# Performance work log

Hardware: AMD Instinct MI355X
Metric: run time of the kernel (lower is better)

Reference implementation:

```python
import jax, jax.numpy as jnp
import numpy as np
from jax import lax

HIDDEN = 256
CONV = 128
DIST = 11
GRID = DIST + 1            # 12
N_STAB = DIST * DIST - 1   # 120
N_LAYERS = 2
DILATIONS = tuple(min(2 ** i, DIST) for i in range(N_LAYERS))  # (1, 2)
EPS = 1e-5

# row-major placement of the first N_STAB grid cells (matches _build_grid_maps)
ROWS = jnp.arange(N_STAB) // GRID
COLS = jnp.arange(N_STAB) % GRID


def setup_inputs() -> dict:
    key = jax.random.key(0)
    ks = jax.random.split(key, 12)
    s_in = 1.0 / np.sqrt(HIDDEN)
    s_cv = 1.0 / np.sqrt(CONV * 9)
    s_out = 1.0 / np.sqrt(CONV)
    return {
        "x": jax.random.normal(ks[0], (4096, N_STAB, HIDDEN), jnp.float32),
        "W_in": jax.random.uniform(ks[1], (HIDDEN, CONV), jnp.float32, -s_in, s_in),
        "b_in": jax.random.uniform(ks[2], (CONV,), jnp.float32, -s_in, s_in),
        "conv_w": jax.random.uniform(ks[3], (N_LAYERS, CONV, CONV, 3, 3), jnp.float32, -s_cv, s_cv),
        "conv_b": jax.random.uniform(ks[4], (N_LAYERS, CONV), jnp.float32, -s_cv, s_cv),
        "bn_g": jnp.ones((N_LAYERS, CONV), jnp.float32),
        "bn_b": jnp.zeros((N_LAYERS, CONV), jnp.float32),
        "W_out": jax.random.uniform(ks[5], (CONV, HIDDEN), jnp.float32, -s_out, s_out),
        "b_out": jax.random.uniform(ks[6], (HIDDEN,), jnp.float32, -s_out, s_out),
        "ln_g": jnp.ones((HIDDEN,), jnp.float32),
        "ln_b": jnp.zeros((HIDDEN,), jnp.float32),
    }


def _dilated_conv(g, w, b, dil):
    # g: [B, C, G, G], w: [O, I, 3, 3]
    y = lax.conv_general_dilated(
        g, w, window_strides=(1, 1),
        padding=((dil, dil), (dil, dil)),
        rhs_dilation=(dil, dil),
        dimension_numbers=("NCHW", "OIHW", "NCHW"))
    return y + b[None, :, None, None]


def _batchnorm_train(y, gamma, beta):
    # training-mode BN: batch stats over (N, H, W), biased variance
    mean = jnp.mean(y, axis=(0, 2, 3), keepdims=True)
    var = jnp.mean(jnp.square(y - mean), axis=(0, 2, 3), keepdims=True)
    yhat = (y - mean) * lax.rsqrt(var + EPS)
    return yhat * gamma[None, :, None, None] + beta[None, :, None, None]


def reference(x, W_in, b_in, conv_w, conv_b, bn_g, bn_b, W_out, b_out, ln_g, ln_b):
    B = x.shape[0]
    # proj_in: [B, S, H] -> [B, S, C]
    h = jnp.einsum("bsh,hc->bsc", x, W_in) + b_in
    # scatter to grid: [B, C, G, G]
    grid = jnp.zeros((B, CONV, GRID, GRID), dtype=h.dtype)
    grid = grid.at[:, :, ROWS, COLS].set(jnp.transpose(h, (0, 2, 1)))
    for i, dil in enumerate(DILATIONS):
        y = _dilated_conv(grid, conv_w[i], conv_b[i], dil)
        grid = grid + jax.nn.relu(_batchnorm_train(y, bn_g[i], bn_b[i]))
    # gather back: [B, S, C]
    h = jnp.transpose(grid[:, :, ROWS, COLS], (0, 2, 1))
    # proj_out + residual + LayerNorm
    h = jnp.einsum("bsc,ch->bsh", h, W_out) + b_out
    z = x + h
    mu = jnp.mean(z, axis=-1, keepdims=True)
    var = jnp.mean(jnp.square(z - mu), axis=-1, keepdims=True)
    return (z - mu) * lax.rsqrt(var + EPS) * ln_g + ln_b
```

## Files before the change

kernel.cpp:

```cpp
#include <hip/hip_runtime.h>

typedef __attribute__((ext_vector_type(8))) unsigned short u16x8;
typedef __attribute__((ext_vector_type(4))) unsigned short u16x4;
typedef __attribute__((ext_vector_type(8))) __bf16 bf16x8;
typedef __attribute__((ext_vector_type(4))) float f32x4;

#define DEVINL __device__ __forceinline__

DEVINL f32x4 MF(u16x8 a, u16x8 b, f32x4 c) {
  return __builtin_amdgcn_mfma_f32_16x16x32_bf16(
      __builtin_bit_cast(bf16x8, a), __builtin_bit_cast(bf16x8, b), c, 0, 0, 0);
}
DEVINL unsigned short f2b(float f) {
  unsigned u = __builtin_bit_cast(unsigned, f);
  u += 0x7FFFu + ((u >> 16) & 1u);
  return (unsigned short)(u >> 16);
}
DEVINL float b2f(unsigned short h) {
  unsigned u = ((unsigned)h) << 16;
  return __builtin_bit_cast(float, u);
}

__global__ void k_prep(const float* __restrict__ W_in, const float* __restrict__ conv_w,
                       const float* __restrict__ W_out, unsigned short* __restrict__ Wt_in,
                       unsigned short* __restrict__ Wc, unsigned short* __restrict__ Wt_out) {
  int t = blockIdx.x * 256 + threadIdx.x;
  if (t < 128 * 256) { int c = t >> 8, h = t & 255; Wt_in[t] = f2b(W_in[h * 128 + c]); }
  if (t < 256 * 128) { int h = t >> 7, c = t & 127; Wt_out[t] = f2b(W_out[c * 256 + h]); }
  for (int i = t; i < 2 * 9 * 128 * 128; i += 65536) {
    int ii = i & 127, o = (i >> 7) & 127, rest = i >> 14;
    int kk = rest % 9, L = rest / 9;
    Wc[i] = f2b(conv_w[(size_t)((L * 128 + o) * 128 + ii) * 9 + kk]);
  }
}

__global__ __launch_bounds__(256) void k_proj_in(
    const float* __restrict__ x, const unsigned short* __restrict__ Wt_in,
    const float* __restrict__ b_in, unsigned short* __restrict__ gridb) {
  __shared__ unsigned short Xb[128 * 256];
  char* XB = (char*)Xb;
  const int b = blockIdx.x;
  const float* xb = x + (size_t)b * 120 * 256;

  for (int idx = threadIdx.x; idx < (120 * 256) / 4; idx += 256) {
    int row = idx >> 6, col = (idx & 63) << 2;
    f32x4 v = *(const f32x4*)(xb + row * 256 + col);
    u16x4 h = { f2b(v[0]), f2b(v[1]), f2b(v[2]), f2b(v[3]) };
    *(u16x4*)(XB + row * 512 + ((col * 2) ^ ((row & 7) << 4))) = h;
  }
  for (int idx = threadIdx.x; idx < (8 * 256) / 4; idx += 256) {
    int row = 120 + (idx >> 6), col = (idx & 63) << 2;
    u16x4 zz = {0, 0, 0, 0};
    *(u16x4*)(XB + row * 512 + ((col * 2) ^ ((row & 7) << 4))) = zz;
  }
  __syncthreads();

  const int l = threadIdx.x & 63, hi = l >> 4, lo = l & 15, w = threadIdx.x >> 6;
  const f32x4 Z = {0.f, 0.f, 0.f, 0.f};
  f32x4 acc[2][8];
#pragma unroll
  for (int a = 0; a < 2; ++a)
#pragma unroll
    for (int n = 0; n < 8; ++n) acc[a][n] = Z;

  const unsigned short* A0 = Wt_in + (w * 32 + lo) * 256;
  const unsigned short* A1 = A0 + 16 * 256;
#pragma unroll
  for (int ks = 0; ks < 8; ++ks) {
    const int kb = ks * 32 + hi * 8;
    u16x8 a0 = *(const u16x8*)(A0 + kb);
    u16x8 a1 = *(const u16x8*)(A1 + kb);
#pragma unroll
    for (int nt = 0; nt < 8; ++nt) {
      int row = nt * 16 + lo;
      u16x8 bf = *(const u16x8*)(XB + row * 512 + ((kb * 2) ^ ((row & 7) << 4)));
      acc[0][nt] = MF(a0, bf, acc[0][nt]);
      acc[1][nt] = MF(a1, bf, acc[1][nt]);
    }
  }

  unsigned short* gb = gridb + (size_t)b * 128 * 144;
#pragma unroll
  for (int am = 0; am < 2; ++am)
#pragma unroll
    for (int r = 0; r < 4; ++r) {
      const int crow = w * 32 + am * 16 + hi * 4 + r;
      const float bias = b_in[crow];
#pragma unroll
      for (int nt = 0; nt < 8; ++nt) {
        int s = nt * 16 + lo;
        if (s < 120) gb[crow * 144 + s] = f2b(acc[am][nt][r] + bias);
      }
    }
  for (int idx = threadIdx.x; idx < 128 * 24; idx += 256) {
    int c = idx / 24, p = idx - c * 24;
    gb[c * 144 + 120 + p] = 0;
  }
}

__global__ __launch_bounds__(256) void k_conv(
    unsigned short* __restrict__ gridb, unsigned short* __restrict__ ybuf,
    const float* __restrict__ statsP, const unsigned short* __restrict__ WcL,
    const float* __restrict__ convbL, float* __restrict__ partials,
    int dil, int writeback) {
  __shared__ unsigned short Gt[145 * 128];
  char* GT = (char*)Gt;
  const int b = blockIdx.x;
  unsigned short* gbp = gridb + (size_t)b * 128 * 144;
  unsigned short* ybp = ybuf + (size_t)b * 128 * 144;

  for (int idx = threadIdx.x; idx < 128 * 18; idx += 256) {
    int c = idx / 18;
    int p0 = (idx - c * 18) * 8;
    u16x8 g = *(const u16x8*)(gbp + c * 144 + p0);
    if (statsP) {
      u16x8 yv = *(const u16x8*)(ybp + c * 144 + p0);
      float a = statsP[c], bb = statsP[128 + c];
#pragma unroll
      for (int j = 0; j < 8; ++j)
        g[j] = f2b(b2f(g[j]) + fmaxf(0.f, b2f(yv[j]) * a + bb));
      if (writeback) *(u16x8*)(gbp + c * 144 + p0) = g;
    }
#pragma unroll
    for (int j = 0; j < 8; ++j) {
      int p = p0 + j;
      *(unsigned short*)(GT + p * 256 + ((c * 2) ^ ((p & 7) << 4))) = g[j];
    }
  }
  if (threadIdx.x < 64) *(unsigned*)(GT + 144 * 256 + threadIdx.x * 4) = 0u;
  __syncthreads();

  const int l = threadIdx.x & 63, hi = l >> 4, lo = l & 15, w = threadIdx.x >> 6;
  const f32x4 Z = {0.f, 0.f, 0.f, 0.f};
  f32x4 acc[2][9];
#pragma unroll
  for (int a = 0; a < 2; ++a)
#pragma unroll
    for (int n = 0; n < 9; ++n) acc[a][n] = Z;

  int pr[9], pc[9];
#pragma unroll
  for (int nt = 0; nt < 9; ++nt) {
    int p = nt * 16 + lo;
    pr[nt] = p / 12;
    pc[nt] = p - pr[nt] * 12;
  }

  for (int off = 0; off < 9; ++off) {
    const int dh = (off / 3 - 1) * dil, dw = (off % 3 - 1) * dil;
    int rb[9], sz[9];
#pragma unroll
    for (int nt = 0; nt < 9; ++nt) {
      int r2 = pr[nt] + dh, c2 = pc[nt] + dw;
      bool ok = ((unsigned)r2 < 12u) && ((unsigned)c2 < 12u);
      int ps = ok ? (r2 * 12 + c2) : 144;
      rb[nt] = ps * 256;
      sz[nt] = (ps & 7) << 4;
    }
    const unsigned short* Ao = WcL + off * (128 * 128);
#pragma unroll
    for (int ks = 0; ks < 4; ++ks) {
      const int kb = ks * 32 + hi * 8;
      u16x8 a0 = *(const u16x8*)(Ao + (w * 32 + lo) * 128 + kb);
      u16x8 a1 = *(const u16x8*)(Ao + (w * 32 + 16 + lo) * 128 + kb);
#pragma unroll
      for (int nt = 0; nt < 9; ++nt) {
        u16x8 bf = *(const u16x8*)(GT + rb[nt] + ((kb * 2) ^ sz[nt]));
        acc[0][nt] = MF(a0, bf, acc[0][nt]);
        acc[1][nt] = MF(a1, bf, acc[1][nt]);
      }
    }
  }

#pragma unroll
  for (int am = 0; am < 2; ++am)
#pragma unroll
    for (int r = 0; r < 4; ++r) {
      const int orow = w * 32 + am * 16 + hi * 4 + r;
      const float bias = convbL[orow];
      float s1 = 0.f, s2 = 0.f;
#pragma unroll
      for (int nt = 0; nt < 9; ++nt) {
        float yv = acc[am][nt][r] + bias;
        s1 += yv; s2 += yv * yv;
        ybp[orow * 144 + nt * 16 + lo] = f2b(yv);
      }
#pragma unroll
      for (int m = 1; m < 16; m <<= 1) { s1 += __shfl_xor(s1, m); s2 += __shfl_xor(s2, m); }
      if (lo == 0) {
        partials[(size_t)orow * 4096 + b] = s1;
        partials[(size_t)(128 + orow) * 4096 + b] = s2;
      }
    }
}

__global__ void k_stats(const float* __restrict__ partials, const float* __restrict__ bn_g,
                        const float* __restrict__ bn_b, float* __restrict__ statsL, float invN) {
  const int c = blockIdx.x, t = threadIdx.x;
  float s1 = 0.f, s2 = 0.f;
  const float* p1 = partials + (size_t)c * 4096;
  const float* p2 = partials + (size_t)(128 + c) * 4096;
  for (int j = t; j < 4096; j += 256) { s1 += p1[j]; s2 += p2[j]; }
#pragma unroll
  for (int m = 1; m < 64; m <<= 1) { s1 += __shfl_xor(s1, m); s2 += __shfl_xor(s2, m); }
  __shared__ float r1[4], r2[4];
  if ((t & 63) == 0) { r1[t >> 6] = s1; r2[t >> 6] = s2; }
  __syncthreads();
  if (t == 0) {
    float S1 = r1[0] + r1[1] + r1[2] + r1[3];
    float S2 = r2[0] + r2[1] + r2[2] + r2[3];
    float mean = S1 * invN;
    float var = fmaxf(S2 * invN - mean * mean, 0.f);
    float a = bn_g[c] * rsqrtf(var + 1e-5f);
    statsL[c] = a;
    statsL[128 + c] = bn_b[c] - mean * a;
  }
}

__global__ __launch_bounds__(256) void k_out(
    const unsigned short* __restrict__ gridb, const unsigned short* __restrict__ ybuf,
    const float* __restrict__ statsP, const unsigned short* __restrict__ Wt_out,
    const float* __restrict__ b_out, const float* __restrict__ x,
    const float* __restrict__ ln_g, const float* __restrict__ ln_b,
    float* __restrict__ out) {
  __shared__ unsigned short Gs[128 * 128];
  char* GT = (char*)Gs;
  const int b = blockIdx.x;
  const unsigned short* gbp = gridb + (size_t)b * 128 * 144;
  const unsigned short* ybp = ybuf + (size_t)b * 128 * 144;

  for (int idx = threadIdx.x; idx < 128 * 15; idx += 256) {
    int c = idx / 15;
    int p0 = (idx - c * 15) * 8;
    u16x8 g = *(const u16x8*)(gbp + c * 144 + p0);
    u16x8 yv = *(const u16x8*)(ybp + c * 144 + p0);
    float a = statsP[c], bb = statsP[128 + c];
#pragma unroll
    for (int j = 0; j < 8; ++j) {
      float v = b2f(g[j]) + fmaxf(0.f, b2f(yv[j]) * a + bb);
      int s = p0 + j;
      *(unsigned short*)(GT + s * 256 + ((c * 2) ^ ((s & 7) << 4))) = f2b(v);
    }
  }
  for (int idx = threadIdx.x; idx < 512; idx += 256)
    *(unsigned*)(GT + 120 * 256 + idx * 4) = 0u;
  __syncthreads();

  const int l = threadIdx.x & 63, hi = l >> 4, lo = l & 15, w = threadIdx.x >> 6;
  const f32x4 Z = {0.f, 0.f, 0.f, 0.f};
  f32x4 acc[2][16];
#pragma unroll
  for (int a = 0; a < 2; ++a)
#pragma unroll
    for (int n = 0; n < 16; ++n) acc[a][n] = Z;

#pragma unroll
  for (int ks = 0; ks < 4; ++ks) {
    const int kb = ks * 32 + hi * 8;
    const int r0 = w * 32 + lo, r1 = r0 + 16;
    u16x8 a0 = *(const u16x8*)(GT + r0 * 256 + ((kb * 2) ^ ((r0 & 7) << 4)));
    u16x8 a1 = *(const u16x8*)(GT + r1 * 256 + ((kb * 2) ^ ((r1 & 7) << 4)));
#pragma unroll
    for (int nt = 0; nt < 16; ++nt) {
      u16x8 bf = *(const u16x8*)(Wt_out + (nt * 16 + lo) * 128 + kb);
      acc[0][nt] = MF(a0, bf, acc[0][nt]);
      acc[1][nt] = MF(a1, bf, acc[1][nt]);
    }
  }

  const float* xb = x + (size_t)b * 120 * 256;
  float* ob = out + (size_t)b * 120 * 256;
#pragma unroll
  for (int am = 0; am < 2; ++am)
#pragma unroll
    for (int r = 0; r < 4; ++r) {
      const int row = w * 32 + am * 16 + hi * 4 + r;
      if (row < 120) {
        float z[16];
        float s1 = 0.f, s2 = 0.f;
#pragma unroll
        for (int nt = 0; nt < 16; ++nt) {
          const int col = nt * 16 + lo;
          float v = acc[am][nt][r] + b_out[col] + xb[row * 256 + col];
          z[nt] = v; s1 += v; s2 += v * v;
        }
#pragma unroll
        for (int m = 1; m < 16; m <<= 1) { s1 += __shfl_xor(s1, m); s2 += __shfl_xor(s2, m); }
        const float mu = s1 * (1.f / 256.f);
        const float var = fmaxf(s2 * (1.f / 256.f) - mu * mu, 0.f);
        const float rs = rsqrtf(var + 1e-5f);
#pragma unroll
        for (int nt = 0; nt < 16; ++nt) {
          const int col = nt * 16 + lo;
          ob[row * 256 + col] = (z[nt] - mu) * rs * ln_g[col] + ln_b[col];
        }
      }
    }
}

extern "C" void kernel_launch(void* const* d_in, const int* in_sizes, int n_in,
                              void* d_out, int out_size, void* d_ws, size_t ws_size,
                              hipStream_t stream) {
  (void)in_sizes; (void)n_in; (void)out_size; (void)ws_size;
  const float* x      = (const float*)d_in[0];
  const float* W_in   = (const float*)d_in[1];
  const float* b_in   = (const float*)d_in[2];
  const float* conv_w = (const float*)d_in[3];
  const float* conv_b = (const float*)d_in[4];
  const float* bn_g   = (const float*)d_in[5];
  const float* bn_b   = (const float*)d_in[6];
  const float* W_out  = (const float*)d_in[7];
  const float* b_out  = (const float*)d_in[8];
  const float* ln_g   = (const float*)d_in[9];
  const float* ln_b   = (const float*)d_in[10];

  char* ws = (char*)d_ws;
  size_t off = 0;
  auto alloc = [&](size_t bytes) { char* p = ws + off; off = (off + bytes + 255) & ~(size_t)255; return p; };
  unsigned short* Wt_in  = (unsigned short*)alloc(128 * 256 * 2);
  unsigned short* Wc     = (unsigned short*)alloc(2 * 9 * 128 * 128 * 2);
  unsigned short* Wt_out = (unsigned short*)alloc(256 * 128 * 2);
  float* stats           = (float*)alloc(2 * 256 * 4);
  float* partials        = (float*)alloc((size_t)256 * 4096 * 4);
  unsigned short* gridb  = (unsigned short*)alloc((size_t)4096 * 128 * 144 * 2);
  unsigned short* ybuf   = (unsigned short*)alloc((size_t)4096 * 128 * 144 * 2);

  const float invN = 1.f / (4096.f * 144.f);

  k_prep<<<256, 256, 0, stream>>>(W_in, conv_w, W_out, Wt_in, Wc, Wt_out);
  k_proj_in<<<4096, 256, 0, stream>>>(x, Wt_in, b_in, gridb);
  k_conv<<<4096, 256, 0, stream>>>(gridb, ybuf, nullptr, Wc, conv_b, partials, 1, 0);
  k_stats<<<128, 256, 0, stream>>>(partials, bn_g, bn_b, stats, invN);
  k_conv<<<4096, 256, 0, stream>>>(gridb, ybuf, stats, Wc + 9 * 128 * 128, conv_b + 128, partials, 2, 1);
  k_stats<<<128, 256, 0, stream>>>(partials, bn_g + 128, bn_b + 128, stats + 256, invN);
  k_out<<<4096, 256, 0, stream>>>(gridb, ybuf, stats + 256, Wt_out, b_out, x, ln_g, ln_b, (float*)d_out);
}
```

Baseline: 1.218 ms.

## Fuse proj_in with first conv and switch grid buffers to position-major layout

Merges the input projection into the first conv kernel so the projected grid stays in shared memory instead of being written out and read back. The grid and conv-output buffers change from channel-major to position-major [144][128], which allows vectorized 16-byte loads and stores in the BN/ReLU prologues. The conv MFMA operands are swapped so that positions form the M dimension, and bf16 conversion now uses the hardware cast. The cost is a more complex fused kernel and possible extra register pressure, and the strided 2-byte y stores remain scattered.

```diff
diff --git a/kernel.cpp b/kernel.cpp
--- a/kernel.cpp
+++ b/kernel.cpp
@@ -1,7 +1,6 @@
 #include <hip/hip_runtime.h>
 
 typedef __attribute__((ext_vector_type(8))) unsigned short u16x8;
-typedef __attribute__((ext_vector_type(4))) unsigned short u16x4;
 typedef __attribute__((ext_vector_type(8))) __bf16 bf16x8;
 typedef __attribute__((ext_vector_type(4))) float f32x4;
 
@@ -12,9 +11,7 @@
       __builtin_bit_cast(bf16x8, a), __builtin_bit_cast(bf16x8, b), c, 0, 0, 0);
 }
 DEVINL unsigned short f2b(float f) {
-  unsigned u = __builtin_bit_cast(unsigned, f);
-  u += 0x7FFFu + ((u >> 16) & 1u);
-  return (unsigned short)(u >> 16);
+  return __builtin_bit_cast(unsigned short, (__bf16)f);
 }
 DEVINL float b2f(unsigned short h) {
   unsigned u = ((unsigned)h) << 16;
@@ -34,164 +31,190 @@
   }
 }
 
-__global__ __launch_bounds__(256) void k_proj_in(
-    const float* __restrict__ x, const unsigned short* __restrict__ Wt_in,
-    const float* __restrict__ b_in, unsigned short* __restrict__ gridb) {
-  __shared__ unsigned short Xb[128 * 256];
-  char* XB = (char*)Xb;
-  const int b = blockIdx.x;
-  const float* xb = x + (size_t)b * 120 * 256;
-
-  for (int idx = threadIdx.x; idx < (120 * 256) / 4; idx += 256) {
-    int row = idx >> 6, col = (idx & 63) << 2;
-    f32x4 v = *(const f32x4*)(xb + row * 256 + col);
-    u16x4 h = { f2b(v[0]), f2b(v[1]), f2b(v[2]), f2b(v[3]) };
-    *(u16x4*)(XB + row * 512 + ((col * 2) ^ ((row & 7) << 4))) = h;
-  }
-  for (int idx = threadIdx.x; idx < (8 * 256) / 4; idx += 256) {
-    int row = 120 + (idx >> 6), col = (idx & 63) << 2;
-    u16x4 zz = {0, 0, 0, 0};
-    *(u16x4*)(XB + row * 512 + ((col * 2) ^ ((row & 7) << 4))) = zz;
-  }
-  __syncthreads();
-
-  const int l = threadIdx.x & 63, hi = l >> 4, lo = l & 15, w = threadIdx.x >> 6;
+DEVINL void conv_body(const char* GT, const unsigned short* __restrict__ WcL,
+                      const float* __restrict__ convbL, int dil,
+                      unsigned short* __restrict__ ybp, float* __restrict__ partials,
+                      int b, int w, int hi, int lo) {
   const f32x4 Z = {0.f, 0.f, 0.f, 0.f};
-  f32x4 acc[2][8];
-#pragma unroll
-  for (int a = 0; a < 2; ++a)
-#pragma unroll
-    for (int n = 0; n < 8; ++n) acc[a][n] = Z;
-
-  const unsigned short* A0 = Wt_in + (w * 32 + lo) * 256;
-  const unsigned short* A1 = A0 + 16 * 256;
-#pragma unroll
-  for (int ks = 0; ks < 8; ++ks) {
-    const int kb = ks * 32 + hi * 8;
-    u16x8 a0 = *(const u16x8*)(A0 + kb);
-    u16x8 a1 = *(const u16x8*)(A1 + kb);
-#pragma unroll
-    for (int nt = 0; nt < 8; ++nt) {
-      int row = nt * 16 + lo;
-      u16x8 bf = *(const u16x8*)(XB + row * 512 + ((kb * 2) ^ ((row & 7) << 4)));
-      acc[0][nt] = MF(a0, bf, acc[0][nt]);
-      acc[1][nt] = MF(a1, bf, acc[1][nt]);
-    }
-  }
-
-  unsigned short* gb = gridb + (size_t)b * 128 * 144;
-#pragma unroll
-  for (int am = 0; am < 2; ++am)
-#pragma unroll
-    for (int r = 0; r < 4; ++r) {
-      const int crow = w * 32 + am * 16 + hi * 4 + r;
-      const float bias = b_in[crow];
-#pragma unroll
-      for (int nt = 0; nt < 8; ++nt) {
-        int s = nt * 16 + lo;
-        if (s < 120) gb[crow * 144 + s] = f2b(acc[am][nt][r] + bias);
-      }
-    }
-  for (int idx = threadIdx.x; idx < 128 * 24; idx += 256) {
-    int c = idx / 24, p = idx - c * 24;
-    gb[c * 144 + 120 + p] = 0;
-  }
-}
-
-__global__ __launch_bounds__(256) void k_conv(
-    unsigned short* __restrict__ gridb, unsigned short* __restrict__ ybuf,
-    const float* __restrict__ statsP, const unsigned short* __restrict__ WcL,
-    const float* __restrict__ convbL, float* __restrict__ partials,
-    int dil, int writeback) {
-  __shared__ unsigned short Gt[145 * 128];
-  char* GT = (char*)Gt;
-  const int b = blockIdx.x;
-  unsigned short* gbp = gridb + (size_t)b * 128 * 144;
-  unsigned short* ybp = ybuf + (size_t)b * 128 * 144;
-
-  for (int idx = threadIdx.x; idx < 128 * 18; idx += 256) {
-    int c = idx / 18;
-    int p0 = (idx - c * 18) * 8;
-    u16x8 g = *(const u16x8*)(gbp + c * 144 + p0);
-    if (statsP) {
-      u16x8 yv = *(const u16x8*)(ybp + c * 144 + p0);
-      float a = statsP[c], bb = statsP[128 + c];
-#pragma unroll
-      for (int j = 0; j < 8; ++j)
-        g[j] = f2b(b2f(g[j]) + fmaxf(0.f, b2f(yv[j]) * a + bb));
-      if (writeback) *(u16x8*)(gbp + c * 144 + p0) = g;
-    }
-#pragma unroll
-    for (int j = 0; j < 8; ++j) {
-      int p = p0 + j;
-      *(unsigned short*)(GT + p * 256 + ((c * 2) ^ ((p & 7) << 4))) = g[j];
-    }
-  }
-  if (threadIdx.x < 64) *(unsigned*)(GT + 144 * 256 + threadIdx.x * 4) = 0u;
-  __syncthreads();
-
-  const int l = threadIdx.x & 63, hi = l >> 4, lo = l & 15, w = threadIdx.x >> 6;
-  const f32x4 Z = {0.f, 0.f, 0.f, 0.f};
-  f32x4 acc[2][9];
-#pragma unroll
-  for (int a = 0; a < 2; ++a)
-#pragma unroll
-    for (int n = 0; n < 9; ++n) acc[a][n] = Z;
+  f32x4 acc[9][2];
+#pragma unroll
+  for (int mt = 0; mt < 9; ++mt) { acc[mt][0] = Z; acc[mt][1] = Z; }
 
   int pr[9], pc[9];
 #pragma unroll
-  for (int nt = 0; nt < 9; ++nt) {
-    int p = nt * 16 + lo;
-    pr[nt] = p / 12;
-    pc[nt] = p - pr[nt] * 12;
+  for (int mt = 0; mt < 9; ++mt) {
+    int p = mt * 16 + lo;
+    pr[mt] = p / 12;
+    pc[mt] = p - pr[mt] * 12;
   }
 
   for (int off = 0; off < 9; ++off) {
     const int dh = (off / 3 - 1) * dil, dw = (off % 3 - 1) * dil;
     int rb[9], sz[9];
 #pragma unroll
-    for (int nt = 0; nt < 9; ++nt) {
-      int r2 = pr[nt] + dh, c2 = pc[nt] + dw;
+    for (int mt = 0; mt < 9; ++mt) {
+      int r2 = pr[mt] + dh, c2 = pc[mt] + dw;
       bool ok = ((unsigned)r2 < 12u) && ((unsigned)c2 < 12u);
       int ps = ok ? (r2 * 12 + c2) : 144;
-      rb[nt] = ps * 256;
-      sz[nt] = (ps & 7) << 4;
+      rb[mt] = ps * 256;
+      sz[mt] = (ps & 7) << 4;
     }
     const unsigned short* Ao = WcL + off * (128 * 128);
 #pragma unroll
     for (int ks = 0; ks < 4; ++ks) {
       const int kb = ks * 32 + hi * 8;
-      u16x8 a0 = *(const u16x8*)(Ao + (w * 32 + lo) * 128 + kb);
-      u16x8 a1 = *(const u16x8*)(Ao + (w * 32 + 16 + lo) * 128 + kb);
-#pragma unroll
-      for (int nt = 0; nt < 9; ++nt) {
-        u16x8 bf = *(const u16x8*)(GT + rb[nt] + ((kb * 2) ^ sz[nt]));
-        acc[0][nt] = MF(a0, bf, acc[0][nt]);
-        acc[1][nt] = MF(a1, bf, acc[1][nt]);
+      u16x8 b0 = *(const u16x8*)(Ao + (w * 32 + lo) * 128 + kb);
+      u16x8 b1 = *(const u16x8*)(Ao + (w * 32 + 16 + lo) * 128 + kb);
+#pragma unroll
+      for (int mt = 0; mt < 9; ++mt) {
+        u16x8 a = *(const u16x8*)(GT + rb[mt] + ((kb * 2) ^ sz[mt]));
+        acc[mt][0] = MF(a, b0, acc[mt][0]);
+        acc[mt][1] = MF(a, b1, acc[mt][1]);
       }
     }
   }
 
-#pragma unroll
-  for (int am = 0; am < 2; ++am)
+  const float bias0 = convbL[w * 32 + lo], bias1 = convbL[w * 32 + 16 + lo];
+  float s1a = 0.f, s2a = 0.f, s1b = 0.f, s2b = 0.f;
+#pragma unroll
+  for (int mt = 0; mt < 9; ++mt)
 #pragma unroll
     for (int r = 0; r < 4; ++r) {
-      const int orow = w * 32 + am * 16 + hi * 4 + r;
-      const float bias = convbL[orow];
-      float s1 = 0.f, s2 = 0.f;
-#pragma unroll
-      for (int nt = 0; nt < 9; ++nt) {
-        float yv = acc[am][nt][r] + bias;
-        s1 += yv; s2 += yv * yv;
-        ybp[orow * 144 + nt * 16 + lo] = f2b(yv);
+      const int p = mt * 16 + hi * 4 + r;
+      float ya = acc[mt][0][r] + bias0;
+      float yb = acc[mt][1][r] + bias1;
+      s1a += ya; s2a += ya * ya; s1b += yb; s2b += yb * yb;
+      ybp[p * 128 + w * 32 + lo]      = f2b(ya);
+      ybp[p * 128 + w * 32 + 16 + lo] = f2b(yb);
+    }
+  s1a += __shfl_xor(s1a, 16); s1a += __shfl_xor(s1a, 32);
+  s2a += __shfl_xor(s2a, 16); s2a += __shfl_xor(s2a, 32);
+  s1b += __shfl_xor(s1b, 16); s1b += __shfl_xor(s1b, 32);
+  s2b += __shfl_xor(s2b, 16); s2b += __shfl_xor(s2b, 32);
+  if (hi == 0) {
+    const int o0 = w * 32 + lo;
+    partials[(size_t)o0 * 4096 + b]              = s1a;
+    partials[(size_t)(128 + o0) * 4096 + b]      = s2a;
+    partials[(size_t)(o0 + 16) * 4096 + b]       = s1b;
+    partials[(size_t)(128 + o0 + 16) * 4096 + b] = s2b;
+  }
+}
+
+__global__ __launch_bounds__(256) void k_in(
+    const float* __restrict__ x, const unsigned short* __restrict__ Wt_in,
+    const float* __restrict__ b_in, const unsigned short* __restrict__ Wc0,
+    const float* __restrict__ convb0, unsigned short* __restrict__ gridb,
+    unsigned short* __restrict__ ybuf, float* __restrict__ partials) {
+  __shared__ unsigned short Gt[145 * 128];
+  char* GT = (char*)Gt;
+  const int b = blockIdx.x, t = threadIdx.x;
+  const int l = t & 63, hi = l >> 4, lo = l & 15, w = t >> 6;
+  const float* xb = x + (size_t)b * 120 * 256;
+
+  const f32x4 Z = {0.f, 0.f, 0.f, 0.f};
+  f32x4 acc[2][8];
+#pragma unroll
+  for (int mi = 0; mi < 2; ++mi)
+#pragma unroll
+    for (int cn = 0; cn < 8; ++cn) acc[mi][cn] = Z;
+
+#pragma unroll
+  for (int ks = 0; ks < 8; ++ks) {
+    const int kb = ks * 32 + hi * 8;
+    u16x8 af[2];
+#pragma unroll
+    for (int mi = 0; mi < 2; ++mi) {
+      int s = w * 32 + mi * 16 + lo;
+      s = s < 120 ? s : 119;
+      const float* px = xb + s * 256 + kb;
+      f32x4 v0 = *(const f32x4*)px;
+      f32x4 v1 = *(const f32x4*)(px + 4);
+      u16x8 a;
+#pragma unroll
+      for (int j = 0; j < 4; ++j) { a[j] = f2b(v0[j]); a[4 + j] = f2b(v1[j]); }
+      af[mi] = a;
+    }
+#pragma unroll
+    for (int cn = 0; cn < 8; ++cn) {
+      u16x8 bf = *(const u16x8*)(Wt_in + (cn * 16 + lo) * 256 + kb);
+      acc[0][cn] = MF(af[0], bf, acc[0][cn]);
+      acc[1][cn] = MF(af[1], bf, acc[1][cn]);
+    }
+  }
+
+  float binr[8];
+#pragma unroll
+  for (int cn = 0; cn < 8; ++cn) binr[cn] = b_in[cn * 16 + lo];
+
+#pragma unroll
+  for (int mi = 0; mi < 2; ++mi)
+#pragma unroll
+    for (int r = 0; r < 4; ++r) {
+      const int s = w * 32 + mi * 16 + hi * 4 + r;
+      if (s < 120) {
+        const int sw = (s & 7) << 4;
+#pragma unroll
+        for (int cn = 0; cn < 8; ++cn) {
+          const int cb = (cn * 16 + lo) * 2;
+          *(unsigned short*)(GT + s * 256 + (cb ^ sw)) = f2b(acc[mi][cn][r] + binr[cn]);
+        }
       }
-#pragma unroll
-      for (int m = 1; m < 16; m <<= 1) { s1 += __shfl_xor(s1, m); s2 += __shfl_xor(s2, m); }
-      if (lo == 0) {
-        partials[(size_t)orow * 4096 + b] = s1;
-        partials[(size_t)(128 + orow) * 4096 + b] = s2;
-      }
-    }
+    }
+  {
+    u16x8 zz = {0, 0, 0, 0, 0, 0, 0, 0};
+    for (int idx = t; idx < 25 * 16; idx += 256) {
+      int row = 120 + (idx >> 4), ch = (idx & 15) << 4;
+      *(u16x8*)(GT + row * 256 + (ch ^ ((row & 7) << 4))) = zz;
+    }
+  }
+  __syncthreads();
+
+  unsigned short* gbp = gridb + (size_t)b * 144 * 128;
+  for (int idx = t; idx < 144 * 16; idx += 256) {
+    int row = idx >> 4, ch = (idx & 15) << 4;
+    u16x8 v = *(const u16x8*)(GT + row * 256 + (ch ^ ((row & 7) << 4)));
+    *(u16x8*)(gbp + row * 128 + ((idx & 15) << 3)) = v;
+  }
+
+  conv_body(GT, Wc0, convb0, 1, ybuf + (size_t)b * 144 * 128, partials, b, w, hi, lo);
+}
+
+__global__ __launch_bounds__(256) void k_conv2(
+    unsigned short* __restrict__ gridb, unsigned short* __restrict__ ybuf,
+    const float* __restrict__ statsP, const unsigned short* __restrict__ WcL,
+    const float* __restrict__ convbL, float* __restrict__ partials) {
+  __shared__ unsigned short Gt[145 * 128];
+  char* GT = (char*)Gt;
+  const int b = blockIdx.x, t = threadIdx.x;
+  unsigned short* gbp = gridb + (size_t)b * 144 * 128;
+  unsigned short* ybp = ybuf + (size_t)b * 144 * 128;
+  const int c0 = (t & 15) * 8, prow = t >> 4;
+  const f32x4 a0 = *(const f32x4*)(statsP + c0);
+  const f32x4 a1 = *(const f32x4*)(statsP + c0 + 4);
+  const f32x4 g0 = *(const f32x4*)(statsP + 128 + c0);
+  const f32x4 g1 = *(const f32x4*)(statsP + 128 + c0 + 4);
+
+#pragma unroll
+  for (int it = 0; it < 9; ++it) {
+    const int p = prow + 16 * it;
+    u16x8 g = *(const u16x8*)(gbp + p * 128 + c0);
+    u16x8 y = *(const u16x8*)(ybp + p * 128 + c0);
+    u16x8 o;
+#pragma unroll
+    for (int j = 0; j < 4; ++j) {
+      o[j]     = f2b(b2f(g[j])     + fmaxf(0.f, b2f(y[j])     * a0[j] + g0[j]));
+      o[4 + j] = f2b(b2f(g[4 + j]) + fmaxf(0.f, b2f(y[4 + j]) * a1[j] + g1[j]));
+    }
+    *(u16x8*)(gbp + p * 128 + c0) = o;
+    *(u16x8*)(GT + p * 256 + ((c0 * 2) ^ ((p & 7) << 4))) = o;
+  }
+  if (t < 16) {
+    u16x8 zz = {0, 0, 0, 0, 0, 0, 0, 0};
+    *(u16x8*)(GT + 144 * 256 + t * 16) = zz;
+  }
+  __syncthreads();
+
+  conv_body(GT, WcL, convbL, 2, ybp, partials, b, t >> 6, (t & 63) >> 4, t & 15);
 }
 
 __global__ void k_stats(const float* __restrict__ partials, const float* __restrict__ bn_g,
@@ -225,63 +248,68 @@
     float* __restrict__ out) {
   __shared__ unsigned short Gs[128 * 128];
   char* GT = (char*)Gs;
-  const int b = blockIdx.x;
-  const unsigned short* gbp = gridb + (size_t)b * 128 * 144;
-  const unsigned short* ybp = ybuf + (size_t)b * 128 * 144;
-
-  for (int idx = threadIdx.x; idx < 128 * 15; idx += 256) {
-    int c = idx / 15;
-    int p0 = (idx - c * 15) * 8;
-    u16x8 g = *(const u16x8*)(gbp + c * 144 + p0);
-    u16x8 yv = *(const u16x8*)(ybp + c * 144 + p0);
-    float a = statsP[c], bb = statsP[128 + c];
-#pragma unroll
-    for (int j = 0; j < 8; ++j) {
-      float v = b2f(g[j]) + fmaxf(0.f, b2f(yv[j]) * a + bb);
-      int s = p0 + j;
-      *(unsigned short*)(GT + s * 256 + ((c * 2) ^ ((s & 7) << 4))) = f2b(v);
-    }
-  }
-  for (int idx = threadIdx.x; idx < 512; idx += 256)
-    *(unsigned*)(GT + 120 * 256 + idx * 4) = 0u;
+  const int b = blockIdx.x, t = threadIdx.x;
+  const unsigned short* gbp = gridb + (size_t)b * 144 * 128;
+  const unsigned short* ybp = ybuf + (size_t)b * 144 * 128;
+  const int c0 = (t & 15) * 8, prow = t >> 4;
+  const f32x4 a0 = *(const f32x4*)(statsP + c0);
+  const f32x4 a1 = *(const f32x4*)(statsP + c0 + 4);
+  const f32x4 g0 = *(const f32x4*)(statsP + 128 + c0);
+  const f32x4 g1 = *(const f32x4*)(statsP + 128 + c0 + 4);
+
+#pragma unroll
+  for (int it = 0; it < 8; ++it) {
+    const int p = prow + 16 * it;
+    u16x8 o = {0, 0, 0, 0, 0, 0, 0, 0};
+    if (p < 120) {
+      u16x8 g = *(const u16x8*)(gbp + p * 128 + c0);
+      u16x8 y = *(const u16x8*)(ybp + p * 128 + c0);
+#pragma unroll
+      for (int j = 0; j < 4; ++j) {
+        o[j]     = f2b(b2f(g[j])     + fmaxf(0.f, b2f(y[j])     * a0[j] + g0[j]));
+        o[4 + j] = f2b(b2f(g[4 + j]) + fmaxf(0.f, b2f(y[4 + j]) * a1[j] + g1[j]));
+      }
+    }
+    *(u16x8*)(GT + p * 256 + ((c0 * 2) ^ ((p & 7) << 4))) = o;
+  }
   __syncthreads();
 
-  const int l = threadIdx.x & 63, hi = l >> 4, lo = l & 15, w = threadIdx.x >> 6;
+  const int l = t & 63, hi = l >> 4, lo = l & 15, w = t >> 6;
   const f32x4 Z = {0.f, 0.f, 0.f, 0.f};
   f32x4 acc[2][16];
 #pragma unroll
-  for (int a = 0; a < 2; ++a)
-#pragma unroll
-    for (int n = 0; n < 16; ++n) acc[a][n] = Z;
+  for (int mi = 0; mi < 2; ++mi)
+#pragma unroll
+    for (int nt = 0; nt < 16; ++nt) acc[mi][nt] = Z;
 
 #pragma unroll
   for (int ks = 0; ks < 4; ++ks) {
     const int kb = ks * 32 + hi * 8;
     const int r0 = w * 32 + lo, r1 = r0 + 16;
-    u16x8 a0 = *(const u16x8*)(GT + r0 * 256 + ((kb * 2) ^ ((r0 & 7) << 4)));
-    u16x8 a1 = *(const u16x8*)(GT + r1 * 256 + ((kb * 2) ^ ((r1 & 7) << 4)));
+    u16x8 A0 = *(const u16x8*)(GT + r0 * 256 + ((kb * 2) ^ ((r0 & 7) << 4)));
+    u16x8 A1 = *(const u16x8*)(GT + r1 * 256 + ((kb * 2) ^ ((r1 & 7) << 4)));
 #pragma unroll
     for (int nt = 0; nt < 16; ++nt) {
       u16x8 bf = *(const u16x8*)(Wt_out + (nt * 16 + lo) * 128 + kb);
-      acc[0][nt] = MF(a0, bf, acc[0][nt]);
-      acc[1][nt] = MF(a1, bf, acc[1][nt]);
+      acc[0][nt] = MF(A0, bf, acc[0][nt]);
+      acc[1][nt] = MF(A1, bf, acc[1][nt]);
     }
   }
 
   const float* xb = x + (size_t)b * 120 * 256;
   float* ob = out + (size_t)b * 120 * 256;
 #pragma unroll
-  for (int am = 0; am < 2; ++am)
+  for (int mi = 0; mi < 2; ++mi)
 #pragma unroll
     for (int r = 0; r < 4; ++r) {
-      const int row = w * 32 + am * 16 + hi * 4 + r;
+      const int row = w * 32 + mi * 16 + hi * 4 + r;
       if (row < 120) {
         float z[16];
         float s1 = 0.f, s2 = 0.f;
 #pragma unroll
         for (int nt = 0; nt < 16; ++nt) {
           const int col = nt * 16 + lo;
-          float v = acc[am][nt][r] + b_out[col] + xb[row * 256 + col];
+          float v = acc[mi][nt][r] + b_out[col] + xb[row * 256 + col];
           z[nt] = v; s1 += v; s2 += v * v;
         }
 #pragma unroll
@@ -322,16 +350,15 @@
   unsigned short* Wt_out = (unsigned short*)alloc(256 * 128 * 2);
   float* stats           = (float*)alloc(2 * 256 * 4);
   float* partials        = (float*)alloc((size_t)256 * 4096 * 4);
-  unsigned short* gridb  = (unsigned short*)alloc((size_t)4096 * 128 * 144 * 2);
-  unsigned short* ybuf   = (unsigned short*)alloc((size_t)4096 * 128 * 144 * 2);
+  unsigned short* gridb  = (unsigned short*)alloc((size_t)4096 * 144 * 128 * 2);
+  unsigned short* ybuf   = (unsigned short*)alloc((size_t)4096 * 144 * 128 * 2);
 
   const float invN = 1.f / (4096.f * 144.f);
 
   k_prep<<<256, 256, 0, stream>>>(W_in, conv_w, W_out, Wt_in, Wc, Wt_out);
-  k_proj_in<<<4096, 256, 0, stream>>>(x, Wt_in, b_in, gridb);
-  k_conv<<<4096, 256, 0, stream>>>(gridb, ybuf, nullptr, Wc, conv_b, partials, 1, 0);
+  k_in<<<4096, 256, 0, stream>>>(x, Wt_in, b_in, Wc, conv_b, gridb, ybuf, partials);
   k_stats<<<128, 256, 0, stream>>>(partials, bn_g, bn_b, stats, invN);
-  k_conv<<<4096, 256, 0, stream>>>(gridb, ybuf, stats, Wc + 9 * 128 * 128, conv_b + 128, partials, 2, 1);
+  k_conv2<<<4096, 256, 0, stream>>>(gridb, ybuf, stats, Wc + 9 * 128 * 128, conv_b + 128, partials);
   k_stats<<<128, 256, 0, stream>>>(partials, bn_g + 128, bn_b + 128, stats + 256, invN);
   k_out<<<4096, 256, 0, stream>>>(gridb, ybuf, stats + 256, Wt_out, b_out, x, ln_g, ln_b, (float*)d_out);
 }
```

After: 1.134 ms. -7.0%, faster.
